# Kernel tuning notes

Hardware: AMD Instinct MI355X
Metric: run time of the kernel (lower is better)

The kernel has to match this reference:

```python
import jax, jax.numpy as jnp
import numpy as np

GROUPS = 32
EPS = 1e-5


def group_norm(x, scale, bias):
    # x: [b, v, t, s, f]; normalize per (b,v,t) sample over (channels_in_group, s)
    b, v, t, s, f = x.shape
    xg = x.reshape(b, v, t, s, GROUPS, f // GROUPS)
    mean = xg.mean(axis=(3, 5), keepdims=True)
    var = xg.var(axis=(3, 5), keepdims=True)
    xn = ((xg - mean) * jax.lax.rsqrt(var + EPS)).reshape(b, v, t, s, f)
    return xn * scale + bias


def nh_conv(x, adjc, W, b):
    # x: [b,v,t,s,f_in]; adjc: [s, k]; W: [k, f_in, f_out]; b: [f_out]
    x_nh = x[:, :, :, adjc, :]                      # [b,v,t,s,k,f_in]
    return jnp.einsum('bvtskf,kfo->bvtso', x_nh, W) + b


def setup_inputs() -> dict:
    key = jax.random.key(0)
    ks = jax.random.split(key, 12)
    B, V, T, S, F_IN, F_OUT, K = 1, 2, 2, 12288, 128, 256, 9
    x = jax.random.normal(ks[0], (B, V, T, S, F_IN), dtype=jnp.float32)
    adjc = jax.random.randint(ks[1], (S, K), 0, S, dtype=jnp.int32)
    gn1_scale = jnp.ones((F_IN,), jnp.float32)
    gn1_bias = jnp.zeros((F_IN,), jnp.float32)
    gn2_scale = jnp.ones((F_OUT,), jnp.float32)
    gn2_bias = jnp.zeros((F_OUT,), jnp.float32)
    W_skip = jax.random.normal(ks[2], (F_IN, F_OUT), jnp.float32) / np.sqrt(F_IN)
    b_skip = jnp.zeros((F_OUT,), jnp.float32)
    W1 = jax.random.normal(ks[3], (K, F_IN, F_OUT), jnp.float32) / np.sqrt(K * F_IN)
    b1 = jnp.zeros((F_OUT,), jnp.float32)
    W2 = jax.random.normal(ks[4], (K, F_OUT, F_OUT), jnp.float32) / np.sqrt(K * F_OUT)
    b2 = jnp.zeros((F_OUT,), jnp.float32)
    return dict(x=x, adjc=adjc, gn1_scale=gn1_scale, gn1_bias=gn1_bias,
                gn2_scale=gn2_scale, gn2_bias=gn2_bias, W_skip=W_skip, b_skip=b_skip,
                W1=W1, b1=b1, W2=W2, b2=b2)


def reference(x, gn1_scale, gn1_bias, gn2_scale, gn2_bias, W_skip, b_skip,
              W1, b1, W2, b2, adjc):
    # skip_layer: ProjLayer with zoom_diff=0 -> plain Linear in->out
    x_res = jnp.einsum('bvtsf,fo->bvtso', x, W_skip) + b_skip
    # norm1 + SiLU (updownconv is Identity when zooms match and in==in feats)
    h = jax.nn.silu(group_norm(x, gn1_scale, gn1_bias))
    # conv1: neighbor-gather linear [k, f_in] -> f_out
    h = nh_conv(h, adjc, W1, b1)
    # emb_layer = Identity; norm2 + SiLU
    h = jax.nn.silu(group_norm(h, gn2_scale, gn2_bias))
    # conv2 + residual
    h = nh_conv(h, adjc, W2, b2)
    return h + x_res
```

## Files before the change

kernel.cpp:

```cpp
#include <hip/hip_runtime.h>
#include <hip/hip_bf16.h>

typedef __bf16 bf16_t;
typedef __bf16 bf16x8 __attribute__((ext_vector_type(8)));
typedef float f32x4 __attribute__((ext_vector_type(4)));
typedef int i32x4 __attribute__((ext_vector_type(4)));

#define S_TOT 12288
#define F_IN 128
#define F_OUT 256
#define EPS 1e-5f

static __device__ __forceinline__ float silu_f(float v) {
  return v / (1.0f + __expf(-v));
}

static __device__ __forceinline__ void gll16(const bf16_t* g, bf16_t* l) {
  __builtin_amdgcn_global_load_lds(
      (const __attribute__((address_space(1))) void*)(const void*)g,
      (__attribute__((address_space(3))) void*)(void*)l, 16, 0, 0);
}

__global__ void prep_kernel(const float* __restrict__ W1,
                            const float* __restrict__ W2,
                            const float* __restrict__ Wsk,
                            bf16_t* __restrict__ W1p,
                            bf16_t* __restrict__ W2p,
                            bf16_t* __restrict__ Wsp,
                            const float* __restrict__ x,
                            float* __restrict__ sum1, float* __restrict__ ss1) {
  __shared__ float gs[32], gq[32];
  if (blockIdx.x < 448) {
    int w = blockIdx.x * 4 + (threadIdx.x >> 6);
    int l = threadIdx.x & 63;
    int lo = l & 15, hi = l >> 4;
    const float* src;
    bf16_t* dst;
    int fbase, obase;
    if (w < 576) {
      int kcg = w >> 4, cb = w & 15;
      int tap = kcg % 9, chunk = kcg / 9;
      src = W1 + tap * 32768;
      dst = W1p + (size_t)w * 512;
      fbase = 32 * chunk + 8 * hi; obase = 16 * cb + lo;
    } else if (w < 1728) {
      int idx = w - 576;
      int kcg = idx >> 4, cb = idx & 15;
      int tap = kcg % 9, chunk = kcg / 9;
      src = W2 + tap * 65536;
      dst = W2p + (size_t)idx * 512;
      fbase = 32 * chunk + 8 * hi; obase = 16 * cb + lo;
    } else {
      int idx = w - 1728;
      int kc = idx >> 4, cb = idx & 15;
      src = Wsk;
      dst = Wsp + (size_t)idx * 512;
      fbase = 32 * kc + 8 * hi; obase = 16 * cb + lo;
    }
    bf16x8 v;
#pragma unroll
    for (int j = 0; j < 8; ++j)
      v[j] = (bf16_t)src[(fbase + j) * 256 + obase];
    *(bf16x8*)(dst + l * 8) = v;
  } else {
    int blk = blockIdx.x - 448;
    int vt = blk & 3;
    int s0 = (blk >> 2) * 256;
    int t = threadIdx.x;
    int col = t & 31, ro = t >> 5;
    float s_ = 0.f, q_ = 0.f;
    const f32x4* xp = (const f32x4*)(x + ((size_t)vt * S_TOT + s0) * F_IN);
#pragma unroll 4
    for (int it = 0; it < 32; ++it) {
      f32x4 v = xp[(size_t)(it * 8 + ro) * 32 + col];
      s_ += v[0] + v[1] + v[2] + v[3];
      q_ += v[0]*v[0] + v[1]*v[1] + v[2]*v[2] + v[3]*v[3];
    }
    if (t < 32) { gs[t] = 0.f; gq[t] = 0.f; }
    __syncthreads();
    atomicAdd(&gs[col], s_);
    atomicAdd(&gq[col], q_);
    __syncthreads();
    if (t < 32) {
      atomicAdd(&sum1[vt * 32 + t], gs[t]);
      atomicAdd(&ss1[vt * 32 + t], gq[t]);
    }
  }
}

__global__ void apply_gn1(const float* __restrict__ x,
                          const float* __restrict__ sum1, const float* __restrict__ ss1,
                          const float* __restrict__ gs, const float* __restrict__ gb,
                          bf16_t* __restrict__ h1) {
  __shared__ float aco[128], bco[128];
  int blk = blockIdx.x;
  int vt = blk / 192;
  size_t base = (size_t)blk * 8192;
  int t = threadIdx.x;
  if (t < 32) {
    float N = (float)(S_TOT * 4);
    float mean = sum1[vt * 32 + t] / N;
    float var = ss1[vt * 32 + t] / N - mean * mean;
    float r = rsqrtf(var + EPS);
#pragma unroll
    for (int j = 0; j < 4; ++j) {
      int c = t * 4 + j;
      float a = r * gs[c];
      aco[c] = a;
      bco[c] = gb[c] - mean * a;
    }
  }
  __syncthreads();
  int c0 = (t * 8) & 127;
  f32x4 A0 = *(const f32x4*)&aco[c0];
  f32x4 A1 = *(const f32x4*)&aco[c0 + 4];
  f32x4 B0 = *(const f32x4*)&bco[c0];
  f32x4 B1 = *(const f32x4*)&bco[c0 + 4];
#pragma unroll
  for (int i = 0; i < 4; ++i) {
    size_t idx = base + (size_t)i * 2048 + t * 8;
    const f32x4* xp = (const f32x4*)(x + idx);
    f32x4 v0 = xp[0], v1 = xp[1];
    bf16x8 o;
#pragma unroll
    for (int j = 0; j < 4; ++j) o[j] = (bf16_t)silu_f(v0[j] * A0[j] + B0[j]);
#pragma unroll
    for (int j = 0; j < 4; ++j) o[4 + j] = (bf16_t)silu_f(v1[j] * A1[j] + B1[j]);
    *(bf16x8*)(h1 + idx) = o;
  }
}

__global__ void apply_gn2(bf16_t* __restrict__ h,
                          const float* __restrict__ sum_c, const float* __restrict__ ss_c,
                          const float* __restrict__ gs, const float* __restrict__ gb) {
  __shared__ float aco[256], bco[256];
  int blk = blockIdx.x;
  int vt = blk / 384;
  size_t base = (size_t)blk * 8192;
  int t = threadIdx.x;
  {
    int c = t;
    int g = c >> 3;
    float sg = 0.f, qg = 0.f;
#pragma unroll
    for (int j = 0; j < 8; ++j) {
      sg += sum_c[vt * 256 + g * 8 + j];
      qg += ss_c[vt * 256 + g * 8 + j];
    }
    float N = (float)(S_TOT * 8);
    float mean = sg / N;
    float var = qg / N - mean * mean;
    float r = rsqrtf(var + EPS);
    float a = r * gs[c];
    aco[c] = a;
    bco[c] = gb[c] - mean * a;
  }
  __syncthreads();
  int c0 = (t * 8) & 255;
  f32x4 A0 = *(const f32x4*)&aco[c0];
  f32x4 A1 = *(const f32x4*)&aco[c0 + 4];
  f32x4 B0 = *(const f32x4*)&bco[c0];
  f32x4 B1 = *(const f32x4*)&bco[c0 + 4];
#pragma unroll
  for (int i = 0; i < 4; ++i) {
    size_t idx = base + (size_t)i * 2048 + t * 8;
    bf16x8 v = *(const bf16x8*)(h + idx);
    bf16x8 o;
#pragma unroll
    for (int j = 0; j < 4; ++j) o[j] = (bf16_t)silu_f((float)v[j] * A0[j] + B0[j]);
#pragma unroll
    for (int j = 0; j < 4; ++j) o[4 + j] = (bf16_t)silu_f((float)v[4 + j] * A1[j] + B1[j]);
    *(bf16x8*)(h + idx) = o;
  }
}

template<int RE, int NM64, bool XSK>
__global__ __launch_bounds__(256, 2) void conv_kernel(
    const bf16_t* __restrict__ hsrc, const bf16_t* __restrict__ Wp,
    const bf16_t* __restrict__ Wsp, const float* __restrict__ x,
    const int* __restrict__ adjc, const float* __restrict__ bias,
    const float* __restrict__ biask, bf16_t* __restrict__ outb,
    float* __restrict__ outf, float* __restrict__ sum_c, float* __restrict__ ss_c) {
  const int tid = threadIdx.x;
  const int wv = tid >> 6, l = tid & 63;
  const int lo = l & 15, hi = l >> 4;
  const int nw = wv;

  int swz = ((blockIdx.x & 7) << 6) + (blockIdx.x >> 3);
  int vt = swz >> 7;
  int rem = swz & 127;
  int s0 = rem * 96;

  __shared__ int adjs[864];
  __shared__ bf16_t ab[3][2][3072];

  for (int i = tid; i < 864; i += 256) adjs[i] = adjc[s0 * 9 + i];
  __syncthreads();

  const bf16_t* hb = hsrc + (size_t)vt * ((size_t)S_TOT * RE);

  auto stageA = [&](int buf, int i) {
    int tap = i % 9, cpair = i / 9;
#pragma unroll
    for (int j2 = 0; j2 < 3; ++j2) {
      int u = wv * 3 + j2;
      int chunk = u / 6, grp = u % 6;
      int row = grp * 16 + (l >> 2);
      int segs = (l & 3) ^ ((row >> 1) & 3);
      const bf16_t* g = hb + (size_t)adjs[row * 9 + tap] * RE + cpair * 64 + chunk * 32 + segs * 8;
      gll16(g, &ab[buf][chunk][grp * 512]);
    }
  };

  auto asmB = [&](i32x4* dst, int i) {
    int tap = i % 9, cpair = i / 9;
    const bf16_t* pa = Wp + (size_t)(18 * cpair + tap) * 8192 + nw * 2048 + l * 8;
    const bf16_t* pb = pa + 9 * 8192;
    asm volatile(
        "global_load_dwordx4 %0, %4, off\n\t"
        "global_load_dwordx4 %1, %4, off offset:1024\n\t"
        "global_load_dwordx4 %2, %4, off offset:2048\n\t"
        "global_load_dwordx4 %3, %4, off offset:3072"
        : "=&v"(dst[0]), "=&v"(dst[1]), "=&v"(dst[2]), "=&v"(dst[3])
        : "v"(pa));
    asm volatile(
        "global_load_dwordx4 %0, %4, off\n\t"
        "global_load_dwordx4 %1, %4, off offset:1024\n\t"
        "global_load_dwordx4 %2, %4, off offset:2048\n\t"
        "global_load_dwordx4 %3, %4, off offset:3072"
        : "=&v"(dst[4]), "=&v"(dst[5]), "=&v"(dst[6]), "=&v"(dst[7])
        : "v"(pb));
  };

  auto asmBx = [&](i32x4* dst, int sx) {
    const bf16_t* pa = Wsp + (size_t)(2 * sx) * 8192 + nw * 2048 + l * 8;
    const bf16_t* pb = pa + 8192;
    asm volatile(
        "global_load_dwordx4 %0, %4, off\n\t"
        "global_load_dwordx4 %1, %4, off offset:1024\n\t"
        "global_load_dwordx4 %2, %4, off offset:2048\n\t"
        "global_load_dwordx4 %3, %4, off offset:3072"
        : "=&v"(dst[0]), "=&v"(dst[1]), "=&v"(dst[2]), "=&v"(dst[3])
        : "v"(pa));
    asm volatile(
        "global_load_dwordx4 %0, %4, off\n\t"
        "global_load_dwordx4 %1, %4, off offset:1024\n\t"
        "global_load_dwordx4 %2, %4, off offset:2048\n\t"
        "global_load_dwordx4 %3, %4, off offset:3072"
        : "=&v"(dst[4]), "=&v"(dst[5]), "=&v"(dst[6]), "=&v"(dst[7])
        : "v"(pb));
  };

  auto stageX = [&](int buf, int sx) {
#pragma unroll
    for (int j = 0; j < 3; ++j) {
      int idx = j * 256 + tid;
      int row = idx >> 3, rest = idx & 7;
      int sc = rest >> 2, q = rest & 3;
      const float* xr = x + ((size_t)vt * S_TOT + s0 + row) * F_IN + sx * 64 + sc * 32 + q * 8;
      f32x4 xv0 = *(const f32x4*)(xr);
      f32x4 xv1 = *(const f32x4*)(xr + 4);
      bf16x8 w;
#pragma unroll
      for (int jj = 0; jj < 4; ++jj) {
        w[jj] = (bf16_t)xv0[jj];
        w[4 + jj] = (bf16_t)xv1[jj];
      }
      *(bf16x8*)(&ab[buf][sc][row * 32 + ((q ^ ((row >> 1) & 3)) << 3)]) = w;
    }
  };

  f32x4 acc[6][4] = {};
  auto compute = [&](int buf, const i32x4* bv) {
    __builtin_amdgcn_s_setprio(1);
#pragma unroll
    for (int sc = 0; sc < 2; ++sc) {
#pragma unroll
      for (int mi = 0; mi < 6; ++mi) {
        int rr = mi * 16 + lo;
        bf16x8 afr = *(const bf16x8*)(&ab[buf][sc][rr * 32 + ((hi ^ ((rr >> 1) & 3)) << 3)]);
#pragma unroll
        for (int ni = 0; ni < 4; ++ni)
          acc[mi][ni] = __builtin_amdgcn_mfma_f32_16x16x32_bf16(
              afr, __builtin_bit_cast(bf16x8, bv[sc * 4 + ni]), acc[mi][ni], 0, 0, 0);
      }
    }
    __builtin_amdgcn_s_setprio(0);
  };

  i32x4 b0[8], b1[8];
  stageA(0, 0);
  asmB(b0, 0);
  stageA(1, 1);
  int bcur3 = 0, bstg3 = 2;

  for (int s = 0; s < NM64 - 2; s += 2) {
    asmB(b1, s + 1);
    asm volatile("s_waitcnt vmcnt(11)" ::: "memory");
    __builtin_amdgcn_s_barrier();
    __builtin_amdgcn_sched_barrier(0);
    stageA(bstg3, s + 2);
    compute(bcur3, b0);
    bcur3 = (bcur3 == 2) ? 0 : bcur3 + 1;
    bstg3 = (bstg3 == 2) ? 0 : bstg3 + 1;
    asmB(b0, s + 2);
    asm volatile("s_waitcnt vmcnt(11)" ::: "memory");
    __builtin_amdgcn_s_barrier();
    __builtin_amdgcn_sched_barrier(0);
    stageA(bstg3, s + 3);
    compute(bcur3, b1);
    bcur3 = (bcur3 == 2) ? 0 : bcur3 + 1;
    bstg3 = (bstg3 == 2) ? 0 : bstg3 + 1;
  }
  asmB(b1, NM64 - 1);
  asm volatile("s_waitcnt vmcnt(11)" ::: "memory");
  __builtin_amdgcn_s_barrier();
  __builtin_amdgcn_sched_barrier(0);
  compute(bcur3, b0);
  bcur3 = (bcur3 == 2) ? 0 : bcur3 + 1;
  asm volatile("s_waitcnt vmcnt(0)" ::: "memory");
  __builtin_amdgcn_s_barrier();
  __builtin_amdgcn_sched_barrier(0);
  compute(bcur3, b1);

  if (XSK) {
#pragma unroll
    for (int sx = 0; sx < 2; ++sx) {
      __syncthreads();
      stageX(sx, sx);
      if (sx) asmBx(b1, sx); else asmBx(b0, sx);
      asm volatile("s_waitcnt vmcnt(0)" ::: "memory");
      __syncthreads();
      __builtin_amdgcn_sched_barrier(0);
      compute(sx, sx ? (const i32x4*)b1 : (const i32x4*)b0);
    }
  }

  if (!XSK) {
    bf16_t* ob = outb + ((size_t)vt * S_TOT + s0) * 256;
#pragma unroll
    for (int ni = 0; ni < 4; ++ni) {
      int o = nw * 64 + ni * 16 + lo;
      float bv = bias[o];
      float s_ = 0.f, q_ = 0.f;
#pragma unroll
      for (int mi = 0; mi < 6; ++mi)
#pragma unroll
        for (int r2 = 0; r2 < 4; ++r2) {
          int srow = mi * 16 + hi * 4 + r2;
          float v = acc[mi][ni][r2] + bv;
          ob[(size_t)srow * 256 + o] = (bf16_t)v;
          s_ += v; q_ += v * v;
        }
      s_ += __shfl_xor(s_, 16); s_ += __shfl_xor(s_, 32);
      q_ += __shfl_xor(q_, 16); q_ += __shfl_xor(q_, 32);
      if (hi == 0) {
        atomicAdd(&sum_c[vt * 256 + o], s_);
        atomicAdd(&ss_c[vt * 256 + o], q_);
      }
    }
  } else {
    float* of = outf + ((size_t)vt * S_TOT + s0) * 256;
#pragma unroll
    for (int ni = 0; ni < 4; ++ni) {
      int o = nw * 64 + ni * 16 + lo;
      float bv = bias[o] + biask[o];
#pragma unroll
      for (int mi = 0; mi < 6; ++mi)
#pragma unroll
        for (int r2 = 0; r2 < 4; ++r2) {
          int srow = mi * 16 + hi * 4 + r2;
          of[(size_t)srow * 256 + o] = acc[mi][ni][r2] + bv;
        }
    }
  }
}

extern "C" void kernel_launch(void* const* d_in, const int* in_sizes, int n_in,
                              void* d_out, int out_size, void* d_ws, size_t ws_size,
                              hipStream_t stream) {
  const float* x      = (const float*)d_in[0];
  const int*   adjc   = (const int*)d_in[1];
  const float* gn1_s  = (const float*)d_in[2];
  const float* gn1_b  = (const float*)d_in[3];
  const float* gn2_s  = (const float*)d_in[4];
  const float* gn2_b  = (const float*)d_in[5];
  const float* W_skip = (const float*)d_in[6];
  const float* b_skip = (const float*)d_in[7];
  const float* W1     = (const float*)d_in[8];
  const float* b1     = (const float*)d_in[9];
  const float* W2     = (const float*)d_in[10];
  const float* b2     = (const float*)d_in[11];
  float* out = (float*)d_out;

  float* sum1  = (float*)d_ws;
  float* ss1   = sum1 + 128;
  float* sum_c = ss1 + 128;
  float* ss_c  = sum_c + 1024;
  float* pad   = ss_c + 1024;
  bf16_t* W1p  = (bf16_t*)(pad + 3072);
  bf16_t* W2p  = W1p + 294912;
  bf16_t* Wsp  = W2p + 589824;
  bf16_t* h1   = Wsp + 32768;
  bf16_t* out1 = h1 + 6291456;

  hipMemsetAsync(sum1, 0, (128 + 128 + 1024 + 1024) * sizeof(float), stream);
  prep_kernel<<<640, 256, 0, stream>>>(W1, W2, W_skip, W1p, W2p, Wsp, x, sum1, ss1);
  apply_gn1<<<768, 256, 0, stream>>>(x, sum1, ss1, gn1_s, gn1_b, h1);
  conv_kernel<128, 18, false><<<512, 256, 0, stream>>>(
      h1, W1p, nullptr, nullptr, adjc, b1, nullptr, out1, nullptr, sum_c, ss_c);
  apply_gn2<<<1536, 256, 0, stream>>>(out1, sum_c, ss_c, gn2_s, gn2_b);
  conv_kernel<256, 36, true><<<512, 256, 0, stream>>>(
      out1, W2p, Wsp, x, adjc, b2, b_skip, nullptr, out, nullptr, nullptr);
}
```

Measured before the change: 128.4 us.

## Fuse group-norm stats and apply via grid barriers into prep and conv1

Merges weight packing, GN1 statistics and GN1 apply into one kernel. Each block keeps its x tile in LDS and waits at a software grid barrier for the global statistics before normalizing. The conv1 epilogue also gains a grid barrier: it accumulates GN2 statistics, waits, then applies GN2+SiLU from registers before writing bf16. This removes two kernel launches plus the extra read and write passes over x and out1. In exchange it relies on all blocks being co-resident (1216 blocks with 32KB LDS each, and 512 conv blocks), which risks deadlock or spin overhead if occupancy falls short.

```diff
diff --git a/kernel.cpp b/kernel.cpp
--- a/kernel.cpp
+++ b/kernel.cpp
@@ -21,18 +21,33 @@
       (__attribute__((address_space(3))) void*)(void*)l, 16, 0, 0);
 }
 
-__global__ void prep_kernel(const float* __restrict__ W1,
-                            const float* __restrict__ W2,
-                            const float* __restrict__ Wsk,
-                            bf16_t* __restrict__ W1p,
-                            bf16_t* __restrict__ W2p,
-                            bf16_t* __restrict__ Wsp,
-                            const float* __restrict__ x,
-                            float* __restrict__ sum1, float* __restrict__ ss1) {
-  __shared__ float gs[32], gq[32];
+static __device__ __forceinline__ void grid_barrier(int* cnt, int n) {
+  __syncthreads();
+  if (threadIdx.x == 0) {
+    __threadfence();
+    __hip_atomic_fetch_add(cnt, 1, __ATOMIC_ACQ_REL, __HIP_MEMORY_SCOPE_AGENT);
+    while (__hip_atomic_load(cnt, __ATOMIC_ACQUIRE, __HIP_MEMORY_SCOPE_AGENT) < n)
+      __builtin_amdgcn_s_sleep(2);
+    __threadfence();
+  }
+  __syncthreads();
+}
+
+__global__ __launch_bounds__(256, 3) void fusedA(
+    const float* __restrict__ W1, const float* __restrict__ W2,
+    const float* __restrict__ Wsk, bf16_t* __restrict__ W1p,
+    bf16_t* __restrict__ W2p, bf16_t* __restrict__ Wsp,
+    const float* __restrict__ x, float* __restrict__ sum1,
+    float* __restrict__ ss1, const float* __restrict__ gs,
+    const float* __restrict__ gb, bf16_t* __restrict__ h1,
+    int* __restrict__ cnt) {
+  __shared__ float sl[8192];
+  __shared__ float gsq[64];
+  __shared__ float aco[128], bco[128];
+  int t = threadIdx.x;
   if (blockIdx.x < 448) {
-    int w = blockIdx.x * 4 + (threadIdx.x >> 6);
-    int l = threadIdx.x & 63;
+    int w = blockIdx.x * 4 + (t >> 6);
+    int l = t & 63;
     int lo = l & 15, hi = l >> 4;
     const float* src;
     bf16_t* dst;
@@ -62,41 +77,30 @@
     for (int j = 0; j < 8; ++j)
       v[j] = (bf16_t)src[(fbase + j) * 256 + obase];
     *(bf16x8*)(dst + l * 8) = v;
-  } else {
-    int blk = blockIdx.x - 448;
-    int vt = blk & 3;
-    int s0 = (blk >> 2) * 256;
-    int t = threadIdx.x;
-    int col = t & 31, ro = t >> 5;
-    float s_ = 0.f, q_ = 0.f;
-    const f32x4* xp = (const f32x4*)(x + ((size_t)vt * S_TOT + s0) * F_IN);
-#pragma unroll 4
-    for (int it = 0; it < 32; ++it) {
-      f32x4 v = xp[(size_t)(it * 8 + ro) * 32 + col];
-      s_ += v[0] + v[1] + v[2] + v[3];
-      q_ += v[0]*v[0] + v[1]*v[1] + v[2]*v[2] + v[3]*v[3];
-    }
-    if (t < 32) { gs[t] = 0.f; gq[t] = 0.f; }
-    __syncthreads();
-    atomicAdd(&gs[col], s_);
-    atomicAdd(&gq[col], q_);
-    __syncthreads();
-    if (t < 32) {
-      atomicAdd(&sum1[vt * 32 + t], gs[t]);
-      atomicAdd(&ss1[vt * 32 + t], gq[t]);
-    }
-  }
-}
-
-__global__ void apply_gn1(const float* __restrict__ x,
-                          const float* __restrict__ sum1, const float* __restrict__ ss1,
-                          const float* __restrict__ gs, const float* __restrict__ gb,
-                          bf16_t* __restrict__ h1) {
-  __shared__ float aco[128], bco[128];
-  int blk = blockIdx.x;
-  int vt = blk / 192;
-  size_t base = (size_t)blk * 8192;
-  int t = threadIdx.x;
+    return;
+  }
+  int b = blockIdx.x - 448;
+  int vt = b / 192;
+  size_t base = (size_t)b * 8192;
+  float s_ = 0.f, q_ = 0.f;
+#pragma unroll
+  for (int i = 0; i < 8; ++i) {
+    int idx = i * 1024 + t * 4;
+    f32x4 v = *(const f32x4*)(x + base + idx);
+    *(f32x4*)&sl[idx] = v;
+    s_ += v[0] + v[1] + v[2] + v[3];
+    q_ += v[0]*v[0] + v[1]*v[1] + v[2]*v[2] + v[3]*v[3];
+  }
+  if (t < 64) gsq[t] = 0.f;
+  __syncthreads();
+  atomicAdd(&gsq[t & 31], s_);
+  atomicAdd(&gsq[32 + (t & 31)], q_);
+  __syncthreads();
+  if (t < 32) {
+    atomicAdd(&sum1[vt * 32 + t], gsq[t]);
+    atomicAdd(&ss1[vt * 32 + t], gsq[32 + t]);
+  }
+  grid_barrier(cnt, 768);
   if (t < 32) {
     float N = (float)(S_TOT * 4);
     float mean = sum1[vt * 32 + t] / N;
@@ -118,59 +122,15 @@
   f32x4 B1 = *(const f32x4*)&bco[c0 + 4];
 #pragma unroll
   for (int i = 0; i < 4; ++i) {
-    size_t idx = base + (size_t)i * 2048 + t * 8;
-    const f32x4* xp = (const f32x4*)(x + idx);
-    f32x4 v0 = xp[0], v1 = xp[1];
+    int idx = i * 2048 + t * 8;
+    f32x4 v0 = *(const f32x4*)&sl[idx];
+    f32x4 v1 = *(const f32x4*)&sl[idx + 4];
     bf16x8 o;
 #pragma unroll
     for (int j = 0; j < 4; ++j) o[j] = (bf16_t)silu_f(v0[j] * A0[j] + B0[j]);
 #pragma unroll
     for (int j = 0; j < 4; ++j) o[4 + j] = (bf16_t)silu_f(v1[j] * A1[j] + B1[j]);
-    *(bf16x8*)(h1 + idx) = o;
-  }
-}
-
-__global__ void apply_gn2(bf16_t* __restrict__ h,
-                          const float* __restrict__ sum_c, const float* __restrict__ ss_c,
-                          const float* __restrict__ gs, const float* __restrict__ gb) {
-  __shared__ float aco[256], bco[256];
-  int blk = blockIdx.x;
-  int vt = blk / 384;
-  size_t base = (size_t)blk * 8192;
-  int t = threadIdx.x;
-  {
-    int c = t;
-    int g = c >> 3;
-    float sg = 0.f, qg = 0.f;
-#pragma unroll
-    for (int j = 0; j < 8; ++j) {
-      sg += sum_c[vt * 256 + g * 8 + j];
-      qg += ss_c[vt * 256 + g * 8 + j];
-    }
-    float N = (float)(S_TOT * 8);
-    float mean = sg / N;
-    float var = qg / N - mean * mean;
-    float r = rsqrtf(var + EPS);
-    float a = r * gs[c];
-    aco[c] = a;
-    bco[c] = gb[c] - mean * a;
-  }
-  __syncthreads();
-  int c0 = (t * 8) & 255;
-  f32x4 A0 = *(const f32x4*)&aco[c0];
-  f32x4 A1 = *(const f32x4*)&aco[c0 + 4];
-  f32x4 B0 = *(const f32x4*)&bco[c0];
-  f32x4 B1 = *(const f32x4*)&bco[c0 + 4];
-#pragma unroll
-  for (int i = 0; i < 4; ++i) {
-    size_t idx = base + (size_t)i * 2048 + t * 8;
-    bf16x8 v = *(const bf16x8*)(h + idx);
-    bf16x8 o;
-#pragma unroll
-    for (int j = 0; j < 4; ++j) o[j] = (bf16_t)silu_f((float)v[j] * A0[j] + B0[j]);
-#pragma unroll
-    for (int j = 0; j < 4; ++j) o[4 + j] = (bf16_t)silu_f((float)v[4 + j] * A1[j] + B1[j]);
-    *(bf16x8*)(h + idx) = o;
+    *(bf16x8*)(h1 + base + idx) = o;
   }
 }
 
@@ -180,7 +140,9 @@
     const bf16_t* __restrict__ Wsp, const float* __restrict__ x,
     const int* __restrict__ adjc, const float* __restrict__ bias,
     const float* __restrict__ biask, bf16_t* __restrict__ outb,
-    float* __restrict__ outf, float* __restrict__ sum_c, float* __restrict__ ss_c) {
+    float* __restrict__ outf, float* __restrict__ sum_c, float* __restrict__ ss_c,
+    const float* __restrict__ g2s, const float* __restrict__ g2b,
+    int* __restrict__ cnt) {
   const int tid = threadIdx.x;
   const int wv = tid >> 6, l = tid & 63;
   const int lo = l & 15, hi = l >> 4;
@@ -337,19 +299,18 @@
   }
 
   if (!XSK) {
-    bf16_t* ob = outb + ((size_t)vt * S_TOT + s0) * 256;
+    float bvv[4];
 #pragma unroll
     for (int ni = 0; ni < 4; ++ni) {
       int o = nw * 64 + ni * 16 + lo;
       float bv = bias[o];
+      bvv[ni] = bv;
       float s_ = 0.f, q_ = 0.f;
 #pragma unroll
       for (int mi = 0; mi < 6; ++mi)
 #pragma unroll
         for (int r2 = 0; r2 < 4; ++r2) {
-          int srow = mi * 16 + hi * 4 + r2;
           float v = acc[mi][ni][r2] + bv;
-          ob[(size_t)srow * 256 + o] = (bf16_t)v;
           s_ += v; q_ += v * v;
         }
       s_ += __shfl_xor(s_, 16); s_ += __shfl_xor(s_, 32);
@@ -358,6 +319,41 @@
         atomicAdd(&sum_c[vt * 256 + o], s_);
         atomicAdd(&ss_c[vt * 256 + o], q_);
       }
+    }
+    grid_barrier(cnt, 512);
+    float* aco = (float*)&ab[0][0][0];
+    float* bco = aco + 256;
+    {
+      int c = tid;
+      int g = c >> 3;
+      float sg = 0.f, qg = 0.f;
+#pragma unroll
+      for (int j = 0; j < 8; ++j) {
+        sg += sum_c[vt * 256 + g * 8 + j];
+        qg += ss_c[vt * 256 + g * 8 + j];
+      }
+      float N = (float)(S_TOT * 8);
+      float mean = sg / N;
+      float var = qg / N - mean * mean;
+      float r = rsqrtf(var + EPS);
+      float a = r * g2s[c];
+      aco[c] = a;
+      bco[c] = g2b[c] - mean * a;
+    }
+    __syncthreads();
+    bf16_t* ob = outb + ((size_t)vt * S_TOT + s0) * 256;
+#pragma unroll
+    for (int ni = 0; ni < 4; ++ni) {
+      int o = nw * 64 + ni * 16 + lo;
+      float a = aco[o], b = bco[o];
+#pragma unroll
+      for (int mi = 0; mi < 6; ++mi)
+#pragma unroll
+        for (int r2 = 0; r2 < 4; ++r2) {
+          int srow = mi * 16 + hi * 4 + r2;
+          float v = acc[mi][ni][r2] + bvv[ni];
+          ob[(size_t)srow * 256 + o] = (bf16_t)silu_f(a * v + b);
+        }
     }
   } else {
     float* of = outf + ((size_t)vt * S_TOT + s0) * 256;
@@ -397,6 +393,7 @@
   float* ss1   = sum1 + 128;
   float* sum_c = ss1 + 128;
   float* ss_c  = sum_c + 1024;
+  int*   cnts  = (int*)(ss_c + 1024);
   float* pad   = ss_c + 1024;
   bf16_t* W1p  = (bf16_t*)(pad + 3072);
   bf16_t* W2p  = W1p + 294912;
@@ -404,12 +401,13 @@
   bf16_t* h1   = Wsp + 32768;
   bf16_t* out1 = h1 + 6291456;
 
-  hipMemsetAsync(sum1, 0, (128 + 128 + 1024 + 1024) * sizeof(float), stream);
-  prep_kernel<<<640, 256, 0, stream>>>(W1, W2, W_skip, W1p, W2p, Wsp, x, sum1, ss1);
-  apply_gn1<<<768, 256, 0, stream>>>(x, sum1, ss1, gn1_s, gn1_b, h1);
+  hipMemsetAsync(sum1, 0, (128 + 128 + 1024 + 1024 + 16) * sizeof(float), stream);
+  fusedA<<<1216, 256, 0, stream>>>(W1, W2, W_skip, W1p, W2p, Wsp,
+                                   x, sum1, ss1, gn1_s, gn1_b, h1, cnts);
   conv_kernel<128, 18, false><<<512, 256, 0, stream>>>(
-      h1, W1p, nullptr, nullptr, adjc, b1, nullptr, out1, nullptr, sum_c, ss_c);
-  apply_gn2<<<1536, 256, 0, stream>>>(out1, sum_c, ss_c, gn2_s, gn2_b);
+      h1, W1p, nullptr, nullptr, adjc, b1, nullptr, out1, nullptr,
+      sum_c, ss_c, gn2_s, gn2_b, cnts + 1);
   conv_kernel<256, 36, true><<<512, 256, 0, stream>>>(
-      out1, W2p, Wsp, x, adjc, b2, b_skip, nullptr, out, nullptr, nullptr);
-}
+      out1, W2p, Wsp, x, adjc, b2, b_skip, nullptr, out,
+      nullptr, nullptr, nullptr, nullptr, nullptr);
+}
```

Result: slower. 259.0 us (+101.6%).

## Fuse GroupNorm2 apply into conv1 epilogue via software grid barrier

Applied to the files above, without the earlier changes.

Conv1 now keeps its accumulators in registers, publishes per-channel sums with atomics, then waits on a software grid-wide barrier. After the barrier it computes the GN2 coefficients and writes the normalized, SiLU-activated bf16 output directly. This removes the separate apply_gn2 kernel and its read-modify-write pass over the 12 MB intermediate. In exchange it relies on all 512 blocks being co-resident (2 blocks per CU under the launch bounds) to avoid deadlock, and it adds spin-wait latency at the barrier.

```diff
diff --git a/kernel.cpp b/kernel.cpp
--- a/kernel.cpp
+++ b/kernel.cpp
@@ -19,6 +19,18 @@
   __builtin_amdgcn_global_load_lds(
       (const __attribute__((address_space(1))) void*)(const void*)g,
       (__attribute__((address_space(3))) void*)(void*)l, 16, 0, 0);
+}
+
+static __device__ __forceinline__ void grid_barrier(int* cnt, int n) {
+  __syncthreads();
+  if (threadIdx.x == 0) {
+    __threadfence();
+    __hip_atomic_fetch_add(cnt, 1, __ATOMIC_ACQ_REL, __HIP_MEMORY_SCOPE_AGENT);
+    while (__hip_atomic_load(cnt, __ATOMIC_ACQUIRE, __HIP_MEMORY_SCOPE_AGENT) < n)
+      __builtin_amdgcn_s_sleep(2);
+    __threadfence();
+  }
+  __syncthreads();
 }
 
 __global__ void prep_kernel(const float* __restrict__ W1,
@@ -130,57 +142,15 @@
   }
 }
 
-__global__ void apply_gn2(bf16_t* __restrict__ h,
-                          const float* __restrict__ sum_c, const float* __restrict__ ss_c,
-                          const float* __restrict__ gs, const float* __restrict__ gb) {
-  __shared__ float aco[256], bco[256];
-  int blk = blockIdx.x;
-  int vt = blk / 384;
-  size_t base = (size_t)blk * 8192;
-  int t = threadIdx.x;
-  {
-    int c = t;
-    int g = c >> 3;
-    float sg = 0.f, qg = 0.f;
-#pragma unroll
-    for (int j = 0; j < 8; ++j) {
-      sg += sum_c[vt * 256 + g * 8 + j];
-      qg += ss_c[vt * 256 + g * 8 + j];
-    }
-    float N = (float)(S_TOT * 8);
-    float mean = sg / N;
-    float var = qg / N - mean * mean;
-    float r = rsqrtf(var + EPS);
-    float a = r * gs[c];
-    aco[c] = a;
-    bco[c] = gb[c] - mean * a;
-  }
-  __syncthreads();
-  int c0 = (t * 8) & 255;
-  f32x4 A0 = *(const f32x4*)&aco[c0];
-  f32x4 A1 = *(const f32x4*)&aco[c0 + 4];
-  f32x4 B0 = *(const f32x4*)&bco[c0];
-  f32x4 B1 = *(const f32x4*)&bco[c0 + 4];
-#pragma unroll
-  for (int i = 0; i < 4; ++i) {
-    size_t idx = base + (size_t)i * 2048 + t * 8;
-    bf16x8 v = *(const bf16x8*)(h + idx);
-    bf16x8 o;
-#pragma unroll
-    for (int j = 0; j < 4; ++j) o[j] = (bf16_t)silu_f((float)v[j] * A0[j] + B0[j]);
-#pragma unroll
-    for (int j = 0; j < 4; ++j) o[4 + j] = (bf16_t)silu_f((float)v[4 + j] * A1[j] + B1[j]);
-    *(bf16x8*)(h + idx) = o;
-  }
-}
-
 template<int RE, int NM64, bool XSK>
 __global__ __launch_bounds__(256, 2) void conv_kernel(
     const bf16_t* __restrict__ hsrc, const bf16_t* __restrict__ Wp,
     const bf16_t* __restrict__ Wsp, const float* __restrict__ x,
     const int* __restrict__ adjc, const float* __restrict__ bias,
     const float* __restrict__ biask, bf16_t* __restrict__ outb,
-    float* __restrict__ outf, float* __restrict__ sum_c, float* __restrict__ ss_c) {
+    float* __restrict__ outf, float* __restrict__ sum_c, float* __restrict__ ss_c,
+    const float* __restrict__ g2s, const float* __restrict__ g2b,
+    int* __restrict__ cnt) {
   const int tid = threadIdx.x;
   const int wv = tid >> 6, l = tid & 63;
   const int lo = l & 15, hi = l >> 4;
@@ -337,19 +307,18 @@
   }
 
   if (!XSK) {
-    bf16_t* ob = outb + ((size_t)vt * S_TOT + s0) * 256;
+    float bvv[4];
 #pragma unroll
     for (int ni = 0; ni < 4; ++ni) {
       int o = nw * 64 + ni * 16 + lo;
       float bv = bias[o];
+      bvv[ni] = bv;
       float s_ = 0.f, q_ = 0.f;
 #pragma unroll
       for (int mi = 0; mi < 6; ++mi)
 #pragma unroll
         for (int r2 = 0; r2 < 4; ++r2) {
-          int srow = mi * 16 + hi * 4 + r2;
           float v = acc[mi][ni][r2] + bv;
-          ob[(size_t)srow * 256 + o] = (bf16_t)v;
           s_ += v; q_ += v * v;
         }
       s_ += __shfl_xor(s_, 16); s_ += __shfl_xor(s_, 32);
@@ -358,6 +327,41 @@
         atomicAdd(&sum_c[vt * 256 + o], s_);
         atomicAdd(&ss_c[vt * 256 + o], q_);
       }
+    }
+    grid_barrier(cnt, 512);
+    float* aco = (float*)&ab[0][0][0];
+    float* bco = aco + 256;
+    {
+      int c = tid;
+      int g = c >> 3;
+      float sg = 0.f, qg = 0.f;
+#pragma unroll
+      for (int j = 0; j < 8; ++j) {
+        sg += sum_c[vt * 256 + g * 8 + j];
+        qg += ss_c[vt * 256 + g * 8 + j];
+      }
+      float N = (float)(S_TOT * 8);
+      float mean = sg / N;
+      float var = qg / N - mean * mean;
+      float r = rsqrtf(var + EPS);
+      float a = r * g2s[c];
+      aco[c] = a;
+      bco[c] = g2b[c] - mean * a;
+    }
+    __syncthreads();
+    bf16_t* ob = outb + ((size_t)vt * S_TOT + s0) * 256;
+#pragma unroll
+    for (int ni = 0; ni < 4; ++ni) {
+      int o = nw * 64 + ni * 16 + lo;
+      float a = aco[o], b = bco[o];
+#pragma unroll
+      for (int mi = 0; mi < 6; ++mi)
+#pragma unroll
+        for (int r2 = 0; r2 < 4; ++r2) {
+          int srow = mi * 16 + hi * 4 + r2;
+          float v = acc[mi][ni][r2] + bvv[ni];
+          ob[(size_t)srow * 256 + o] = (bf16_t)silu_f(a * v + b);
+        }
     }
   } else {
     float* of = outf + ((size_t)vt * S_TOT + s0) * 256;
@@ -397,6 +401,7 @@
   float* ss1   = sum1 + 128;
   float* sum_c = ss1 + 128;
   float* ss_c  = sum_c + 1024;
+  int*   cnts  = (int*)(ss_c + 1024);
   float* pad   = ss_c + 1024;
   bf16_t* W1p  = (bf16_t*)(pad + 3072);
   bf16_t* W2p  = W1p + 294912;
@@ -404,12 +409,13 @@
   bf16_t* h1   = Wsp + 32768;
   bf16_t* out1 = h1 + 6291456;
 
-  hipMemsetAsync(sum1, 0, (128 + 128 + 1024 + 1024) * sizeof(float), stream);
+  hipMemsetAsync(sum1, 0, (128 + 128 + 1024 + 1024 + 16) * sizeof(float), stream);
   prep_kernel<<<640, 256, 0, stream>>>(W1, W2, W_skip, W1p, W2p, Wsp, x, sum1, ss1);
   apply_gn1<<<768, 256, 0, stream>>>(x, sum1, ss1, gn1_s, gn1_b, h1);
   conv_kernel<128, 18, false><<<512, 256, 0, stream>>>(
-      h1, W1p, nullptr, nullptr, adjc, b1, nullptr, out1, nullptr, sum_c, ss_c);
-  apply_gn2<<<1536, 256, 0, stream>>>(out1, sum_c, ss_c, gn2_s, gn2_b);
+      h1, W1p, nullptr, nullptr, adjc, b1, nullptr, out1, nullptr,
+      sum_c, ss_c, gn2_s, gn2_b, cnts);
   conv_kernel<256, 36, true><<<512, 256, 0, stream>>>(
-      out1, W2p, Wsp, x, adjc, b2, b_skip, nullptr, out, nullptr, nullptr);
-}
+      out1, W2p, Wsp, x, adjc, b2, b_skip, nullptr, out,
+      nullptr, nullptr, nullptr, nullptr, nullptr);
+}
```

New measurement: 177.1 us. 37.9% more time.
